# Performance work log

Measured on AMD Instinct MI355X. Metric: run time of the kernel, lower is better.

Reference implementation:

```python
import jax, jax.numpy as jnp
import numpy as np

N, E, IN, HID, OUT, H, G = 50000, 800000, 128, 32, 32, 4, 64
NEG_SLOPE = 0.2


def setup_inputs() -> dict:
    key = jax.random.key(0)
    ks = jax.random.split(key, 12)
    p = lambda k, s: jax.random.normal(k, s, jnp.float32) * 0.1
    x = jax.random.normal(ks[0], (N, IN), jnp.float32)
    edge_index = jax.random.randint(ks[1], (2, E), 0, N, dtype=jnp.int64)
    batch = jnp.sort(jax.random.randint(ks[2], (N,), 0, G, dtype=jnp.int64))
    return {
        'x': x, 'edge_index': edge_index, 'batch': batch,
        'W1': p(ks[3], (IN, H * HID)),
        'att_src1': p(ks[4], (H, HID)), 'att_dst1': p(ks[5], (H, HID)),
        'b1': jnp.zeros((H * HID,), jnp.float32),
        'W2': p(ks[6], (H * HID, H * OUT)),
        'att_src2': p(ks[7], (H, OUT)), 'att_dst2': p(ks[8], (H, OUT)),
        'b2': jnp.zeros((H * OUT,), jnp.float32),
        'lin_w': p(ks[9], (H * OUT, 1)),
        'lin_b': jnp.zeros((1,), jnp.float32),
    }


def gat_conv(x, src, dst, W, a_src, a_dst, b, heads, ch):
    # x: [N, F_in]; src/dst: [E'] with self-loops already appended.
    n = x.shape[0]
    h = (x @ W).reshape(n, heads, ch)                      # [N, H, C]
    alpha_s = jnp.einsum('nhc,hc->nh', h, a_src)           # [N, H]
    alpha_d = jnp.einsum('nhc,hc->nh', h, a_dst)
    e = jax.nn.leaky_relu(alpha_s[src] + alpha_d[dst], NEG_SLOPE)  # [E', H]
    # segment softmax over destination neighborhoods
    m = jax.ops.segment_max(e, dst, num_segments=n)
    m = jnp.where(jnp.isfinite(m), m, 0.0)
    ex = jnp.exp(e - m[dst])
    s = jax.ops.segment_sum(ex, dst, num_segments=n)
    alpha = ex / (s[dst] + 1e-16)                          # [E', H]
    out = jax.ops.segment_sum(alpha[:, :, None] * h[src], dst, num_segments=n)
    return out.reshape(n, heads * ch) + b


def reference(x, edge_index, batch, W1, att_src1, att_dst1, b1,
              W2, att_src2, att_dst2, b2, lin_w, lin_b):
    # add self-loops (PyG GATConv default add_self_loops=True)
    loops = jnp.arange(N, dtype=edge_index.dtype)
    src = jnp.concatenate([edge_index[0], loops])
    dst = jnp.concatenate([edge_index[1], loops])

    h = jax.nn.elu(gat_conv(x, src, dst, W1, att_src1, att_dst1, b1, H, HID))
    h = gat_conv(h, src, dst, W2, att_src2, att_dst2, b2, H, OUT)  # [N, H*OUT]

    # global mean + max pool per graph
    counts = jax.ops.segment_sum(jnp.ones((N,), h.dtype), batch, num_segments=G)
    mean_p = jax.ops.segment_sum(h, batch, num_segments=G) / jnp.maximum(counts, 1.0)[:, None]
    max_p = jax.ops.segment_max(h, batch, num_segments=G)
    max_p = jnp.where(jnp.isfinite(max_p), max_p, 0.0)
    pooled = mean_p + max_p                                # [G, H*OUT]
    return pooled @ lin_w + lin_b                          # [G, 1]
```

## Files before the change

kernel.cpp:

```cpp
#include <hip/hip_runtime.h>
#include <hip/hip_bf16.h>
#include <hip/hip_fp16.h>
#include <math.h>

#define NEG_SLOPE 0.2f
#define BCAP 64
#define LAYER_W 18432

typedef _Float16 half8 __attribute__((ext_vector_type(8)));
typedef _Float16 half4v __attribute__((ext_vector_type(4)));
typedef float f32x4 __attribute__((ext_vector_type(4)));


__device__ __forceinline__ int lbound(const int* __restrict__ a, int n, int key) {
    int lo = 0, hi = n;
    while (lo < hi) {
        int mid = (lo + hi) >> 1;
        if (a[mid] < key) lo = mid + 1; else hi = mid;
    }
    return lo;
}

__device__ __forceinline__ unsigned encf(float f) {
    unsigned u = __float_as_uint(f);
    return (u & 0x80000000u) ? ~u : (u | 0x80000000u);
}
__device__ __forceinline__ float decf(unsigned u) {
    return (u & 0x80000000u) ? __uint_as_float(u & 0x7FFFFFFFu) : __uint_as_float(~u);
}


__global__ void init_kernel(int* __restrict__ cnt, unsigned short* __restrict__ col,
                            float* __restrict__ gsum, unsigned* __restrict__ gmax,
                            int n, int gtot) {
    int i = blockIdx.x * blockDim.x + threadIdx.x;
    if (i < n) {
        cnt[i] = 1;
        col[(size_t)i * BCAP] = (unsigned short)i;
    }
    if (i < gtot) { gsum[i] = 0.f; gmax[i] = 0x007FFFFFu;  }
}

__global__ void build_kernel(const int* __restrict__ src, const int* __restrict__ dst,
                             int* __restrict__ cnt, unsigned short* __restrict__ col, int E) {
    int i = blockIdx.x * blockDim.x + threadIdx.x;
    if (i >= E) return;
    int d = dst[i];
    int slot = atomicAdd(&cnt[d], 1);
    if (slot < BCAP) col[(size_t)d * BCAP + slot] = (unsigned short)src[i];
}


__global__ void wprep_kernel(const float* __restrict__ W1, const float* __restrict__ W2,
                             const float* __restrict__ as1, const float* __restrict__ ad1,
                             const float* __restrict__ as2, const float* __restrict__ ad2,
                             _Float16* __restrict__ wt_hi, _Float16* __restrict__ wt_lo) {
    int b = blockIdx.x;
    int layer = b / 36;
    int rem = b % 36;
    int nt = rem >> 2;
    int kc = rem & 3;
    const float* W  = layer ? W2 : W1;
    const float* As = layer ? as2 : as1;
    const float* Ad = layer ? ad2 : ad1;
    int lane = threadIdx.x;
    int n = lane & 15, q = lane >> 4;
    size_t base = (size_t)layer * LAYER_W + (size_t)((nt * 4 + kc) * 64 + lane) * 8;
    #pragma unroll
    for (int j = 0; j < 8; ++j) {
        int k = kc * 32 + q * 8 + j;
        float w = 0.f;
        if (nt < 8) {
            w = W[(size_t)k * 128 + nt * 16 + n];
        } else if (n < 4) {
            for (int c = 0; c < 32; ++c) w += W[(size_t)k * 128 + n * 32 + c] * As[n * 32 + c];
        } else if (n < 8) {
            int hh = n - 4;
            for (int c = 0; c < 32; ++c) w += W[(size_t)k * 128 + hh * 32 + c] * Ad[hh * 32 + c];
        }
        _Float16 hi = (_Float16)w;
        wt_hi[base + j] = hi;
        wt_lo[base + j] = (_Float16)(w - (float)hi);
    }
}


__global__ __launch_bounds__(256) void gemm_attn_kernel(
        const float* __restrict__ A,
        const _Float16* __restrict__ wt_hi, const _Float16* __restrict__ wt_lo,
        _Float16* __restrict__ H16, float* __restrict__ as_, float* __restrict__ ad_,
        int M) {
    __shared__ _Float16 a_hi[64][136];

    int tid = threadIdx.x;
    int m0 = blockIdx.x * 64;

    #pragma unroll
    for (int t = 0; t < 8; ++t) {
        int f = tid + t * 256;
        int r = f >> 5;
        int c4 = (f & 31) << 2;
        int gr = m0 + r; if (gr >= M) gr = M - 1;
        const float4 v = *(const float4*)(A + (size_t)gr * 128 + c4);
        half4v hi = { (_Float16)v.x, (_Float16)v.y, (_Float16)v.z, (_Float16)v.w };
        *(half4v*)&a_hi[r][c4] = hi;
    }
    __syncthreads();

    int w = tid >> 6;
    int lane = tid & 63;
    int cbase = lane & 15;
    int q = lane >> 4;
    int mrow = (w << 4) + cbase;

    f32x4 acc[9];
    #pragma unroll
    for (int nt = 0; nt < 9; ++nt) acc[nt] = (f32x4){0.f, 0.f, 0.f, 0.f};

    #pragma unroll
    for (int kc = 0; kc < 4; ++kc) {
        half8 ah = *(half8*)&a_hi[mrow][kc * 32 + q * 8];
        #pragma unroll
        for (int nt = 0; nt < 9; ++nt) {
            const half8 bh = *(const half8*)(wt_hi + (size_t)((nt * 4 + kc) * 64 + lane) * 8);
            const half8 bl = *(const half8*)(wt_lo + (size_t)((nt * 4 + kc) * 64 + lane) * 8);
            acc[nt] = __builtin_amdgcn_mfma_f32_16x16x32_f16(ah, bh, acc[nt], 0, 0, 0);
            acc[nt] = __builtin_amdgcn_mfma_f32_16x16x32_f16(ah, bl, acc[nt], 0, 0, 0);
        }
    }

    #pragma unroll
    for (int nt = 0; nt < 8; ++nt) {
        int c = nt * 16 + cbase;
        #pragma unroll
        for (int i = 0; i < 4; ++i) {
            int gr = m0 + (w << 4) + (q << 2) + i;
            if (gr < M) H16[(size_t)gr * 128 + c] = (_Float16)acc[nt][i];
        }
    }
    if (cbase < 8) {
        #pragma unroll
        for (int i = 0; i < 4; ++i) {
            int gr = m0 + (w << 4) + (q << 2) + i;
            if (gr < M) {
                if (cbase < 4) as_[(size_t)gr * 4 + cbase]     = acc[8][i];
                else           ad_[(size_t)gr * 4 + cbase - 4] = acc[8][i];
            }
        }
    }
}


__global__ __launch_bounds__(256) void agg_kernel(
        const int* __restrict__ cnt, const unsigned short* __restrict__ col,
        const _Float16* __restrict__ h16, const float* __restrict__ as_,
        const float* __restrict__ ad_, const float* __restrict__ bias,
        float* __restrict__ out, int n, int elu) {
    __shared__ int   s_col[4][64];
    __shared__ float s_w[4][256];

    int wvb  = threadIdx.x >> 6;
    int lane = threadIdx.x & 63;
    int wv   = blockIdx.x * 4 + wvb;
    int valid = (wv < n);
    if (!valid) wv = n - 1;

    int deg = cnt[wv]; if (deg > BCAP) deg = BCAP;
    const unsigned short* crow = col + (size_t)wv * BCAP;
    const float4 adv = *(const float4*)(ad_ + (size_t)wv * 4);

    int q = lane >> 4;
    int r = lane & 15;
    int head = r >> 2;
    const _Float16* hrow = h16 + 8 * r;

    if (lane < deg) {
        int s = crow[lane];
        const float4 av = *(const float4*)(as_ + (size_t)s * 4);
        float e0 = av.x + adv.x, e1 = av.y + adv.y;
        float e2 = av.z + adv.z, e3 = av.w + adv.w;
        float w0 = __expf(fmaxf(e0, NEG_SLOPE * e0));
        float w1 = __expf(fmaxf(e1, NEG_SLOPE * e1));
        float w2 = __expf(fmaxf(e2, NEG_SLOPE * e2));
        float w3 = __expf(fmaxf(e3, NEG_SLOPE * e3));
        s_col[wvb][lane] = s;
        *(float4*)&s_w[wvb][lane * 4] = make_float4(w0, w1, w2, w3);
    } else {
        s_col[wvb][lane] = 0;
        *(float4*)&s_w[wvb][lane * 4] = make_float4(0.f, 0.f, 0.f, 0.f);
    }
    __syncthreads();

    float lsum = 0.f;
    float acc[8];
    #pragma unroll
    for (int j = 0; j < 8; ++j) acc[j] = 0.f;

    for (int it = 0; it < deg; it += 16) {
        int ea = it + q;
        int eb = ea + 4;
        int ec = ea + 8;
        int ed = ea + 12;
        int sa = s_col[wvb][ea];
        int sb = s_col[wvb][eb];
        int sc = s_col[wvb][ec];
        int sd = s_col[wvb][ed];
        float wa = s_w[wvb][ea * 4 + head];
        float wb = s_w[wvb][eb * 4 + head];
        float wc = s_w[wvb][ec * 4 + head];
        float wd = s_w[wvb][ed * 4 + head];
        const half8 ha = *(const half8*)(hrow + (size_t)sa * 128);
        const half8 hb = *(const half8*)(hrow + (size_t)sb * 128);
        const half8 hc = *(const half8*)(hrow + (size_t)sc * 128);
        const half8 hd = *(const half8*)(hrow + (size_t)sd * 128);
        lsum += wa + wb + wc + wd;
        #pragma unroll
        for (int j = 0; j < 8; ++j)
            acc[j] += wa * (float)ha[j] + wb * (float)hb[j]
                    + wc * (float)hc[j] + wd * (float)hd[j];
    }

    #pragma unroll
    for (int j = 0; j < 8; ++j) {
        acc[j] += __shfl_xor(acc[j], 16, 64);
        acc[j] += __shfl_xor(acc[j], 32, 64);
    }
    lsum += __shfl_xor(lsum, 16, 64);
    lsum += __shfl_xor(lsum, 32, 64);

    if (lane < 16 && valid) {
        float inv = 1.f / (lsum + 1e-16f);
        const float4 bv0 = *(const float4*)(bias + 8 * r);
        const float4 bv1 = *(const float4*)(bias + 8 * r + 4);
        float o[8];
        o[0] = acc[0] * inv + bv0.x; o[1] = acc[1] * inv + bv0.y;
        o[2] = acc[2] * inv + bv0.z; o[3] = acc[3] * inv + bv0.w;
        o[4] = acc[4] * inv + bv1.x; o[5] = acc[5] * inv + bv1.y;
        o[6] = acc[6] * inv + bv1.z; o[7] = acc[7] * inv + bv1.w;
        if (elu) {
            #pragma unroll
            for (int j = 0; j < 8; ++j) o[j] = o[j] > 0.f ? o[j] : expm1f(o[j]);
        }
        *(float4*)(out + (size_t)wv * 128 + 8 * r)     = make_float4(o[0], o[1], o[2], o[3]);
        *(float4*)(out + (size_t)wv * 128 + 8 * r + 4) = make_float4(o[4], o[5], o[6], o[7]);
    }
}


__global__ void pool1_kernel(const float* __restrict__ h, const int* __restrict__ batch,
                             float* __restrict__ gsum, unsigned* __restrict__ gmax, int n) {
    int g = blockIdx.x >> 3;
    int p = blockIdx.x & 7;
    int c = threadIdx.x;
    int s = lbound(batch, n, g);
    int e = lbound(batch, n, g + 1);
    int len = e - s;
    int lo = s + (int)((long long)len * p / 8);
    int hi = s + (int)((long long)len * (p + 1) / 8);
    float sum = 0.f, mx = -INFINITY;
    for (int i = lo; i < hi; ++i) {
        float v = h[(size_t)i * 128 + c];
        sum += v; mx = fmaxf(mx, v);
    }
    if (hi > lo) {
        atomicAdd(&gsum[g * 128 + c], sum);
        atomicMax(&gmax[g * 128 + c], encf(mx));
    }
}

__global__ void pool2_kernel(const float* __restrict__ gsum, const unsigned* __restrict__ gmax,
                             const int* __restrict__ batch, const float* __restrict__ lin_w,
                             const float* __restrict__ lin_b, float* __restrict__ out, int n) {
    int g = blockIdx.x;
    int c = threadIdx.x;
    int s = lbound(batch, n, g);
    int e = lbound(batch, n, g + 1);
    float cnt = fmaxf((float)(e - s), 1.0f);
    float mean = gsum[g * 128 + c] / cnt;
    float mx = decf(gmax[g * 128 + c]);
    if (!isfinite(mx)) mx = 0.f;
    float v = (mean + mx) * lin_w[c];
    __shared__ float red[128];
    red[c] = v;
    __syncthreads();
    for (int off = 64; off > 0; off >>= 1) {
        if (c < off) red[c] += red[c + off];
        __syncthreads();
    }
    if (c == 0) out[g] = red[0] + lin_b[0];
}


extern "C" void kernel_launch(void* const* d_in, const int* in_sizes, int n_in,
                              void* d_out, int out_size, void* d_ws, size_t ws_size,
                              hipStream_t stream) {
    const float* x    = (const float*)d_in[0];
    const int*   ei   = (const int*)d_in[1];
    const int*   batch= (const int*)d_in[2];
    const float* W1   = (const float*)d_in[3];
    const float* at_s1= (const float*)d_in[4];
    const float* at_d1= (const float*)d_in[5];
    const float* b1   = (const float*)d_in[6];
    const float* W2   = (const float*)d_in[7];
    const float* at_s2= (const float*)d_in[8];
    const float* at_d2= (const float*)d_in[9];
    const float* b2   = (const float*)d_in[10];
    const float* lw   = (const float*)d_in[11];
    const float* lb   = (const float*)d_in[12];
    float* out = (float*)d_out;

    const int N = in_sizes[0] / 128;
    const int E = in_sizes[1] / 2;
    const int G = out_size;

    char* p = (char*)d_ws;
    auto carve = [&](size_t bytes) -> void* {
        void* q = (void*)p;
        p += (bytes + 255) & ~(size_t)255;
        return q;
    };
    _Float16*       h16   = (_Float16*)carve((size_t)N * 128 * 2);
    float*          agg   = (float*)carve((size_t)N * 128 * 4);
    float*          asb   = (float*)carve((size_t)N * 4 * 4);
    float*          adb   = (float*)carve((size_t)N * 4 * 4);
    int*            cnt   = (int*)carve((size_t)N * 4);
    unsigned short* col   = (unsigned short*)carve((size_t)N * BCAP * 2);
    float*          gsum  = (float*)carve((size_t)G * 128 * 4);
    unsigned*       gmax  = (unsigned*)carve((size_t)G * 128 * 4);
    _Float16*       wt_hi = (_Float16*)carve((size_t)2 * LAYER_W * 2);
    _Float16*       wt_lo = (_Float16*)carve((size_t)2 * LAYER_W * 2);

    const int* esrc = ei;
    const int* edst = ei + E;

    int initN = (N > G * 128) ? N : G * 128;
    init_kernel<<<(initN + 255) / 256, 256, 0, stream>>>(cnt, col, gsum, gmax, N, G * 128);
    build_kernel<<<(E + 255) / 256, 256, 0, stream>>>(esrc, edst, cnt, col, E);
    wprep_kernel<<<72, 64, 0, stream>>>(W1, W2, at_s1, at_d1, at_s2, at_d2, wt_hi, wt_lo);

    gemm_attn_kernel<<<(N + 63) / 64, 256, 0, stream>>>(
        x, wt_hi, wt_lo, h16, asb, adb, N);
    agg_kernel<<<(N + 3) / 4, 256, 0, stream>>>(cnt, col, h16, asb, adb, b1, agg, N, 1);

    gemm_attn_kernel<<<(N + 63) / 64, 256, 0, stream>>>(
        agg, wt_hi + LAYER_W, wt_lo + LAYER_W, h16, asb, adb, N);
    agg_kernel<<<(N + 3) / 4, 256, 0, stream>>>(cnt, col, h16, asb, adb, b2, agg, N, 0);

    pool1_kernel<<<G * 8, 128, 0, stream>>>(agg, batch, gsum, gmax, N);
    pool2_kernel<<<G, 128, 0, stream>>>(gsum, gmax, batch, lw, lb, out, N);
}
```

Before: 294.7 us.

## Partition adjacency build by destination range across XCDs and drop init kernel

The adjacency build kernel now launches 8 blocks per edge chunk. Each block keeps only edges whose destination falls in one eighth of the node range, so atomics and scattered column writes stay within one slice of memory, which plausibly maps to one XCD's L2 under round-robin block dispatch. Self-loops are no longer stored; the aggregation kernel adds the node itself as an implicit last neighbour. The init kernel is replaced with memsets. In exchange, each block re-reads the destination array eight times and the graph-max buffer now starts at encoded zero instead of the encoded negative infinity.

After: 291.3 us. Within noise of the previous version (-1.1%).

```diff
diff --git a/kernel.cpp b/kernel.cpp
--- a/kernel.cpp
+++ b/kernel.cpp
@@ -30,24 +30,19 @@
 }
 
 
-__global__ void init_kernel(int* __restrict__ cnt, unsigned short* __restrict__ col,
-                            float* __restrict__ gsum, unsigned* __restrict__ gmax,
-                            int n, int gtot) {
-    int i = blockIdx.x * blockDim.x + threadIdx.x;
-    if (i < n) {
-        cnt[i] = 1;
-        col[(size_t)i * BCAP] = (unsigned short)i;
-    }
-    if (i < gtot) { gsum[i] = 0.f; gmax[i] = 0x007FFFFFu;  }
-}
-
 __global__ void build_kernel(const int* __restrict__ src, const int* __restrict__ dst,
-                             int* __restrict__ cnt, unsigned short* __restrict__ col, int E) {
-    int i = blockIdx.x * blockDim.x + threadIdx.x;
+                             int* __restrict__ cnt, unsigned short* __restrict__ col,
+                             int E, int n) {
+    int part  = blockIdx.x & 7;
+    int chunk = blockIdx.x >> 3;
+    int i = chunk * 256 + threadIdx.x;
     if (i >= E) return;
     int d = dst[i];
+    int psz = (n + 7) >> 3;
+    int lo = part * psz;
+    if (d < lo || d >= lo + psz) return;
     int slot = atomicAdd(&cnt[d], 1);
-    if (slot < BCAP) col[(size_t)d * BCAP + slot] = (unsigned short)src[i];
+    if (slot < BCAP - 1) col[(size_t)d * BCAP + slot] = (unsigned short)src[i];
 }
 
 
@@ -165,7 +160,8 @@
     int valid = (wv < n);
     if (!valid) wv = n - 1;
 
-    int deg = cnt[wv]; if (deg > BCAP) deg = BCAP;
+    int degr = cnt[wv]; if (degr > BCAP - 1) degr = BCAP - 1;
+    int deg = degr + 1;
     const unsigned short* crow = col + (size_t)wv * BCAP;
     const float4 adv = *(const float4*)(ad_ + (size_t)wv * 4);
 
@@ -175,7 +171,7 @@
     const _Float16* hrow = h16 + 8 * r;
 
     if (lane < deg) {
-        int s = crow[lane];
+        int s = (lane == degr) ? wv : (int)crow[lane];
         const float4 av = *(const float4*)(as_ + (size_t)s * 4);
         float e0 = av.x + adv.x, e1 = av.y + adv.y;
         float e2 = av.z + adv.z, e3 = av.w + adv.w;
@@ -333,9 +329,12 @@
     const int* esrc = ei;
     const int* edst = ei + E;
 
-    int initN = (N > G * 128) ? N : G * 128;
-    init_kernel<<<(initN + 255) / 256, 256, 0, stream>>>(cnt, col, gsum, gmax, N, G * 128);
-    build_kernel<<<(E + 255) / 256, 256, 0, stream>>>(esrc, edst, cnt, col, E);
+    hipMemsetAsync(cnt,  0, (size_t)N * 4, stream);
+    hipMemsetAsync(gsum, 0, (size_t)G * 128 * 4, stream);
+    hipMemsetAsync(gmax, 0, (size_t)G * 128 * 4, stream);
+
+    const int nchunk = (E + 255) / 256;
+    build_kernel<<<nchunk * 8, 256, 0, stream>>>(esrc, edst, cnt, col, E, N);
     wprep_kernel<<<72, 64, 0, stream>>>(W1, W2, at_s1, at_d1, at_s2, at_d2, wt_hi, wt_lo);
 
     gemm_attn_kernel<<<(N + 63) / 64, 256, 0, stream>>>(
```
